# Performance work log

Measured on AMD Instinct MI355X. Metric: run time of the kernel, lower is better.

Reference implementation:

```python
import jax, jax.numpy as jnp
import numpy as np

D_MODEL = 1024

def setup_inputs() -> dict:
    key = jax.random.key(0)
    ks = jax.random.split(key, 5)
    s = 1.0 / np.sqrt(D_MODEL)  # torch Linear default init scale-ish
    x = jax.random.normal(ks[0], (4, 2048, D_MODEL), dtype=jnp.float32)
    Wq = jax.random.normal(ks[1], (D_MODEL, D_MODEL), dtype=jnp.float32) * s
    Wk = jax.random.normal(ks[2], (D_MODEL, D_MODEL), dtype=jnp.float32) * s
    Wv = jax.random.normal(ks[3], (D_MODEL, D_MODEL), dtype=jnp.float32) * s
    Wo = jax.random.normal(ks[4], (D_MODEL, D_MODEL), dtype=jnp.float32) * s
    z = jnp.zeros((D_MODEL,), dtype=jnp.float32)
    return {"x": x, "Wq": Wq, "bq": z, "Wk": Wk, "bk": z, "Wv": Wv, "bv": z, "Wo": Wo, "bo": z}

def reference(x, Wq, bq, Wk, bk, Wv, bv, Wo, bo):
    # x: (B, S, D). Single-head causal attention, dropout in eval mode (identity).
    B, S, D = x.shape
    Q = jnp.einsum('bsd,ed->bse', x, Wq) + bq
    K = jnp.einsum('bsd,ed->bse', x, Wk) + bk
    V = jnp.einsum('bsd,ed->bse', x, Wv) + bv
    scores = jnp.einsum('bqd,bkd->bqk', Q, K) / jnp.sqrt(jnp.float32(D))
    causal = jnp.tril(jnp.ones((S, S), dtype=bool))  # (S, S)
    scores = jnp.where(causal, scores, -jnp.inf)
    weights = jax.nn.softmax(scores, axis=-1)
    attended = jnp.einsum('bqk,bkd->bqd', weights, V)
    out = jnp.einsum('bsd,ed->bse', attended, Wo) + bo
    return out
```

## Files before the change

### kernel.cpp

```cpp
#include <hip/hip_runtime.h>
#include <cstdint>
#include <cstddef>


#define D_MODEL 1024
#define SEQ     2048
#define BATCH   4

typedef unsigned short u16;
typedef __bf16 bf16_t;
typedef bf16_t bf16x8 __attribute__((ext_vector_type(8)));
typedef float  f32x4  __attribute__((ext_vector_type(4)));
typedef u16    u16x4  __attribute__((ext_vector_type(4)));

__device__ __forceinline__ u16 f2bf(float x) {
  union { float f; uint32_t u; } v; v.f = x;
  uint32_t r = v.u + 0x7fffu + ((v.u >> 16) & 1u);
  return (u16)(r >> 16);
}

__device__ __forceinline__ void gload_lds16(const u16* g, u16* l) {
  __builtin_amdgcn_global_load_lds((__attribute__((address_space(1))) void*)g,
                                   (__attribute__((address_space(3))) void*)l,
                                   16, 0, 0);
}

template <bool ROWSUM>
__device__ __forceinline__ void gemm_core(const u16* __restrict__ Ablk,
                                          const u16* __restrict__ Bblk,
                                          int lda, int ldb, int ksteps64,
                                          u16* As, u16* Bs,
                                          f32x4 acc[4][4], f32x4* rs) {
  const int tid  = threadIdx.x;
  const int wave = tid >> 6, lane = tid & 63;
  const int wr = (wave >> 1) * 64, wc = (wave & 1) * 64;
  const int frow = lane & 15, kq = lane >> 4;
  int sm[4], sk[4];
#pragma unroll
  for (int t = 0; t < 4; ++t) {
    const int ch = t * 256 + tid;
    sm[t] = ch >> 3;
    sk[t] = ((ch & 7) ^ (sm[t] & 7)) * 8;
  }
  int aoff[4], boff[4];
#pragma unroll
  for (int i = 0; i < 4; ++i) {
    const int ra = wr + i * 16 + frow;
    aoff[i] = ra * 64 + ((kq ^ (ra & 7)) * 8);
    const int rb = wc + i * 16 + frow;
    boff[i] = rb * 64 + ((kq ^ (rb & 7)) * 8);
  }
  bf16x8 ones;
  if (ROWSUM) {
#pragma unroll
    for (int r = 0; r < 8; ++r) ((u16*)&ones)[r] = 0x3F80;
  }

  for (int kt = 0; kt < ksteps64; ++kt) {
    __syncthreads();
    const int kb = kt * 64;
#pragma unroll
    for (int t = 0; t < 4; ++t)
      gload_lds16(Ablk + sm[t] * lda + kb + sk[t], As + (t * 256 + tid) * 8);
#pragma unroll
    for (int t = 0; t < 4; ++t)
      gload_lds16(Bblk + sm[t] * ldb + kb + sk[t], Bs + (t * 256 + tid) * 8);
    asm volatile("s_waitcnt vmcnt(0)" ::: "memory");
    __syncthreads();

#pragma unroll
    for (int kh = 0; kh < 2; ++kh) {
      const int xo = kh * 32;
      bf16x8 af[4], bf[4];
#pragma unroll
      for (int i = 0; i < 4; ++i) af[i] = *(const bf16x8*)(As + (aoff[i] ^ xo));
#pragma unroll
      for (int j = 0; j < 4; ++j) bf[j] = *(const bf16x8*)(Bs + (boff[j] ^ xo));
#pragma unroll
      for (int i = 0; i < 4; ++i)
#pragma unroll
        for (int j = 0; j < 4; ++j)
          acc[i][j] = __builtin_amdgcn_mfma_f32_16x16x32_bf16(af[i], bf[j], acc[i][j], 0, 0, 0);
      if (ROWSUM) {
#pragma unroll
        for (int i = 0; i < 4; ++i)
          rs[i] = __builtin_amdgcn_mfma_f32_16x16x32_bf16(af[i], ones, rs[i], 0, 0, 0);
      }
    }
  }
}

__global__ __launch_bounds__(256) void cvt_kernel(const float4* __restrict__ x,
                                                  const float4* __restrict__ wq,
                                                  const float4* __restrict__ wk,
                                                  const float4* __restrict__ wv,
                                                  const float4* __restrict__ wo,
                                                  u16* __restrict__ dst) {
  const int i = blockIdx.x * 256 + threadIdx.x;
  float4 v;
  if (i < 2097152) {
    v = x[i];
  } else {
    const int j = i - 2097152;
    const int w = j >> 18;
    const float4* s = (w == 0) ? wq : (w == 1) ? wk : (w == 2) ? wv : wo;
    v = s[j & 262143];
  }
  u16x4 o = {f2bf(v.x), f2bf(v.y), f2bf(v.z), f2bf(v.w)};
  *(u16x4*)(dst + (size_t)i * 4) = o;
}

__global__ __launch_bounds__(256) void proj_qk_kernel(const u16* __restrict__ xb,
                                                      const u16* __restrict__ Wq,
                                                      const u16* __restrict__ Wk,
                                                      const float* __restrict__ bq,
                                                      const float* __restrict__ bk,
                                                      u16* __restrict__ Qb,
                                                      u16* __restrict__ Kb) {
  __shared__ __align__(16) u16 As[128 * 64];
  __shared__ __align__(16) u16 Bs[128 * 64];
  const int z = blockIdx.z;
  const u16*   W    = z ? Wk : Wq;
  const float* bias = z ? bk : bq;
  u16*         out  = z ? Kb : Qb;
  const int row0 = blockIdx.x * 128, col0 = blockIdx.y * 128;
  f32x4 acc[4][4] = {};
  gemm_core<false>(xb + (size_t)row0 * D_MODEL, W + (size_t)col0 * D_MODEL,
                   D_MODEL, D_MODEL, 16, As, Bs, acc, nullptr);
  const int lane = threadIdx.x & 63, wave = threadIdx.x >> 6;
  const int wr = (wave >> 1) * 64, wc = (wave & 1) * 64;
  const int cl = lane & 15, rl = (lane >> 4) * 4;
#pragma unroll
  for (int j = 0; j < 4; ++j) {
    const int col = col0 + wc + j * 16 + cl;
    const float bb = bias[col];
#pragma unroll
    for (int i = 0; i < 4; ++i)
#pragma unroll
      for (int r = 0; r < 4; ++r) {
        const int row = row0 + wr + i * 16 + rl + r;
        out[(size_t)row * D_MODEL + col] = f2bf(acc[i][j][r] + bb);
      }
  }
}

__global__ __launch_bounds__(256) void proj_v_kernel(const u16* __restrict__ xb,
                                                     const u16* __restrict__ Wv,
                                                     const float* __restrict__ bv,
                                                     u16* __restrict__ Vt) {
  __shared__ __align__(16) u16 As[128 * 64];
  __shared__ __align__(16) u16 Bs[128 * 64];
  const int row0 = blockIdx.x * 128, col0 = blockIdx.y * 128;
  f32x4 acc[4][4] = {};
  gemm_core<false>(xb + (size_t)row0 * D_MODEL, Wv + (size_t)col0 * D_MODEL,
                   D_MODEL, D_MODEL, 16, As, Bs, acc, nullptr);
  const int lane = threadIdx.x & 63, wave = threadIdx.x >> 6;
  const int wr = (wave >> 1) * 64, wc = (wave & 1) * 64;
  const int cl = lane & 15, rl = (lane >> 4) * 4;
  const int b = row0 >> 11;
  u16* vt = Vt + (size_t)b * D_MODEL * SEQ;
#pragma unroll
  for (int j = 0; j < 4; ++j) {
    const int col = col0 + wc + j * 16 + cl;
    const float bb = bv[col];
#pragma unroll
    for (int i = 0; i < 4; ++i) {
      const int s0 = (row0 & 2047) + wr + i * 16 + rl;
      u16x4 o = {f2bf(acc[i][j][0] + bb), f2bf(acc[i][j][1] + bb),
                 f2bf(acc[i][j][2] + bb), f2bf(acc[i][j][3] + bb)};
      *(u16x4*)(vt + (size_t)col * SEQ + s0) = o;
    }
  }
}

__global__ __launch_bounds__(256) void scores_kernel(const u16* __restrict__ Qb,
                                                     const u16* __restrict__ Kb,
                                                     u16* __restrict__ Eb) {
  const int t = blockIdx.x, b = blockIdx.z;
  int qi = (int)((sqrtf(8.0f * t + 1.0f) - 1.0f) * 0.5f);
  if ((qi + 1) * (qi + 2) / 2 <= t) ++qi;
  if (qi * (qi + 1) / 2 > t) --qi;
  const int ji = t - qi * (qi + 1) / 2;
  __shared__ __align__(16) u16 As[128 * 64];
  __shared__ __align__(16) u16 Bs[128 * 64];
  const u16* A  = Qb + (size_t)(b * SEQ + qi * 128) * D_MODEL;
  const u16* Bt = Kb + (size_t)(b * SEQ + ji * 128) * D_MODEL;
  f32x4 acc[4][4] = {};
  gemm_core<false>(A, Bt, D_MODEL, D_MODEL, 16, As, Bs, acc, nullptr);
  u16* out = Eb + (size_t)b * SEQ * SEQ;
  const int lane = threadIdx.x & 63, wave = threadIdx.x >> 6;
  const int wr = (wave >> 1) * 64, wc = (wave & 1) * 64;
  const int cl = lane & 15, rl = (lane >> 4) * 4;
#pragma unroll
  for (int i = 0; i < 4; ++i)
#pragma unroll
    for (int r = 0; r < 4; ++r) {
      const int q = qi * 128 + wr + i * 16 + rl + r;
#pragma unroll
      for (int j = 0; j < 4; ++j) {
        const int jj = ji * 128 + wc + j * 16 + cl;
        out[(size_t)q * SEQ + jj] =
            (jj <= q) ? f2bf(__expf(acc[i][j][r] * 0.03125f)) : (u16)0;
      }
    }
}

__global__ __launch_bounds__(256) void pv_kernel(const u16* __restrict__ Eb,
                                                 const u16* __restrict__ Vt,
                                                 u16* __restrict__ Ab) {
  __shared__ __align__(16) u16 As[128 * 64];
  __shared__ __align__(16) u16 Bs[128 * 64];
  const int qt = 15 - blockIdx.x, dt = blockIdx.y, b = blockIdx.z;
  const u16* A  = Eb + (size_t)b * SEQ * SEQ + (size_t)(qt * 128) * SEQ;
  const u16* Bt = Vt + (size_t)b * D_MODEL * SEQ + (size_t)(dt * 128) * SEQ;
  f32x4 acc[4][4] = {};
  f32x4 rs[4] = {};
  gemm_core<true>(A, Bt, SEQ, SEQ, (qt + 1) * 2, As, Bs, acc, rs);
  const int lane = threadIdx.x & 63, wave = threadIdx.x >> 6;
  const int wr = (wave >> 1) * 64, wc = (wave & 1) * 64;
  const int cl = lane & 15, rl = (lane >> 4) * 4;
#pragma unroll
  for (int i = 0; i < 4; ++i)
#pragma unroll
    for (int r = 0; r < 4; ++r) {
      const float invl = 1.0f / rs[i][r];
      const int row = b * SEQ + qt * 128 + wr + i * 16 + rl + r;
#pragma unroll
      for (int j = 0; j < 4; ++j) {
        const int col = dt * 128 + wc + j * 16 + cl;
        Ab[(size_t)row * D_MODEL + col] = f2bf(acc[i][j][r] * invl);
      }
    }
}

__global__ __launch_bounds__(256) void out_kernel(const u16* __restrict__ Ab,
                                                  const u16* __restrict__ Wo,
                                                  const float* __restrict__ bo,
                                                  float* __restrict__ Out) {
  __shared__ __align__(16) u16 As[128 * 64];
  __shared__ __align__(16) u16 Bs[128 * 64];
  const int row0 = blockIdx.x * 128, col0 = blockIdx.y * 128;
  f32x4 acc[4][4] = {};
  gemm_core<false>(Ab + (size_t)row0 * D_MODEL, Wo + (size_t)col0 * D_MODEL,
                   D_MODEL, D_MODEL, 16, As, Bs, acc, nullptr);
  const int lane = threadIdx.x & 63, wave = threadIdx.x >> 6;
  const int wr = (wave >> 1) * 64, wc = (wave & 1) * 64;
  const int cl = lane & 15, rl = (lane >> 4) * 4;
#pragma unroll
  for (int j = 0; j < 4; ++j) {
    const int col = col0 + wc + j * 16 + cl;
    const float bb = bo[col];
#pragma unroll
    for (int i = 0; i < 4; ++i)
#pragma unroll
      for (int r = 0; r < 4; ++r) {
        const int row = row0 + wr + i * 16 + rl + r;
        Out[(size_t)row * D_MODEL + col] = acc[i][j][r] + bb;
      }
  }
}

extern "C" void kernel_launch(void* const* d_in, const int* in_sizes, int n_in,
                              void* d_out, int out_size, void* d_ws, size_t ws_size,
                              hipStream_t stream) {
  const float* x  = (const float*)d_in[0];
  const float* Wq = (const float*)d_in[1];
  const float* bq = (const float*)d_in[2];
  const float* Wk = (const float*)d_in[3];
  const float* bk = (const float*)d_in[4];
  const float* Wv = (const float*)d_in[5];
  const float* bv = (const float*)d_in[6];
  const float* Wo = (const float*)d_in[7];
  const float* bo = (const float*)d_in[8];
  float* out = (float*)d_out;
  char* ws = (char*)d_ws;

  u16* xb = (u16*)(ws);
  u16* Wb = (u16*)(ws + (16u << 20));
  u16* Qb = (u16*)(ws + (24u << 20));
  u16* Kb = (u16*)(ws + (40u << 20));
  u16* Vt = (u16*)(ws + (56u << 20));
  u16* Eb = (u16*)(ws + (72u << 20));
  u16* Ab = (u16*)(ws + (104u << 20));

  cvt_kernel<<<12288, 256, 0, stream>>>((const float4*)x, (const float4*)Wq,
                                        (const float4*)Wk, (const float4*)Wv,
                                        (const float4*)Wo, xb);
  proj_qk_kernel<<<dim3(64, 8, 2), 256, 0, stream>>>(xb, Wb, Wb + (1u << 20),
                                                     bq, bk, Qb, Kb);
  proj_v_kernel<<<dim3(64, 8), 256, 0, stream>>>(xb, Wb + (2u << 20), bv, Vt);
  scores_kernel<<<dim3(136, 1, 4), 256, 0, stream>>>(Qb, Kb, Eb);
  pv_kernel<<<dim3(16, 8, 4), 256, 0, stream>>>(Eb, Vt, Ab);
  out_kernel<<<dim3(64, 8), 256, 0, stream>>>(Ab, Wb + (3u << 20), bo, out);
}
```

Baseline: 291.2 us.

## Fold output projection into V weights and merge stages into fewer kernels

Precomputes Wp = Wo·Wv and bp = Wo·bv so that V' = x·Wpᵀ + bp already includes the output projection. The separate out_kernel GEMM is removed and pv_kernel writes the final fp32 output plus bo directly. The QK projections are merged with the Wp computation into one launch, and the scores GEMM with the V' projection into another, to cut launch count and fill more of the GPU. The cost is an extra 1024³ weight GEMM, a transpose and an added bf16 rounding of the fused weight, which can shift accuracy.

```diff
diff --git a/kernel.cpp b/kernel.cpp
--- a/kernel.cpp
+++ b/kernel.cpp
@@ -110,104 +110,148 @@
   *(u16x4*)(dst + (size_t)i * 4) = o;
 }
 
-__global__ __launch_bounds__(256) void proj_qk_kernel(const u16* __restrict__ xb,
-                                                      const u16* __restrict__ Wq,
-                                                      const u16* __restrict__ Wk,
-                                                      const float* __restrict__ bq,
-                                                      const float* __restrict__ bk,
-                                                      u16* __restrict__ Qb,
-                                                      u16* __restrict__ Kb) {
+__global__ void transposeW_kernel(const u16* __restrict__ src, u16* __restrict__ dst) {
+  __shared__ u16 tile[32][33];
+  const int r0 = blockIdx.x * 32, c0 = blockIdx.y * 32;
+  const int tx = threadIdx.x, ty = threadIdx.y;
+#pragma unroll
+  for (int r = 0; r < 4; ++r)
+    tile[ty + r * 8][tx] = src[(size_t)(r0 + ty + r * 8) * D_MODEL + c0 + tx];
+  __syncthreads();
+#pragma unroll
+  for (int r = 0; r < 4; ++r)
+    dst[(size_t)(c0 + ty + r * 8) * D_MODEL + r0 + tx] = tile[tx][ty + r * 8];
+}
+
+__global__ __launch_bounds__(256) void stageA_kernel(
+    const u16* __restrict__ xb,
+    const u16* __restrict__ WqB, const u16* __restrict__ WkB,
+    const u16* __restrict__ WoB, const u16* __restrict__ WvT,
+    const float* __restrict__ Wo32, const float* __restrict__ bv,
+    const float* __restrict__ bq, const float* __restrict__ bk,
+    u16* __restrict__ Qb, u16* __restrict__ Kb,
+    u16* __restrict__ Wp, float* __restrict__ bp) {
   __shared__ __align__(16) u16 As[128 * 64];
   __shared__ __align__(16) u16 Bs[128 * 64];
-  const int z = blockIdx.z;
-  const u16*   W    = z ? Wk : Wq;
-  const float* bias = z ? bk : bq;
-  u16*         out  = z ? Kb : Qb;
-  const int row0 = blockIdx.x * 128, col0 = blockIdx.y * 128;
-  f32x4 acc[4][4] = {};
-  gemm_core<false>(xb + (size_t)row0 * D_MODEL, W + (size_t)col0 * D_MODEL,
-                   D_MODEL, D_MODEL, 16, As, Bs, acc, nullptr);
+  const int blk = blockIdx.x;
   const int lane = threadIdx.x & 63, wave = threadIdx.x >> 6;
   const int wr = (wave >> 1) * 64, wc = (wave & 1) * 64;
   const int cl = lane & 15, rl = (lane >> 4) * 4;
-#pragma unroll
-  for (int j = 0; j < 4; ++j) {
-    const int col = col0 + wc + j * 16 + cl;
-    const float bb = bias[col];
-#pragma unroll
-    for (int i = 0; i < 4; ++i)
-#pragma unroll
-      for (int r = 0; r < 4; ++r) {
-        const int row = row0 + wr + i * 16 + rl + r;
-        out[(size_t)row * D_MODEL + col] = f2bf(acc[i][j][r] + bb);
-      }
-  }
-}
-
-__global__ __launch_bounds__(256) void proj_v_kernel(const u16* __restrict__ xb,
-                                                     const u16* __restrict__ Wv,
-                                                     const float* __restrict__ bv,
-                                                     u16* __restrict__ Vt) {
+
+  if (blk < 64) {
+    const int f0 = (blk >> 3) * 128, e0 = (blk & 7) * 128;
+    f32x4 acc[4][4] = {};
+    gemm_core<false>(WoB + (size_t)f0 * D_MODEL, WvT + (size_t)e0 * D_MODEL,
+                     D_MODEL, D_MODEL, 16, As, Bs, acc, nullptr);
+#pragma unroll
+    for (int j = 0; j < 4; ++j) {
+      const int col = e0 + wc + j * 16 + cl;
+#pragma unroll
+      for (int i = 0; i < 4; ++i)
+#pragma unroll
+        for (int r = 0; r < 4; ++r) {
+          const int row = f0 + wr + i * 16 + rl + r;
+          Wp[(size_t)row * D_MODEL + col] = f2bf(acc[i][j][r]);
+        }
+    }
+  } else if (blk < 80) {
+    const int f = (blk - 64) * 64 + (threadIdx.x >> 2);
+    const int dq = threadIdx.x & 3;
+    const float* row = Wo32 + (size_t)f * D_MODEL + dq * 256;
+    const float* bvq = bv + dq * 256;
+    float s = 0.f;
+#pragma unroll 8
+    for (int i = 0; i < 256; ++i) s += row[i] * bvq[i];
+    s += __shfl_xor(s, 1);
+    s += __shfl_xor(s, 2);
+    if (dq == 0) bp[f] = s;
+  } else {
+    const int u = blk - 80;
+    const int z = u >> 9;
+    const u16*   W    = z ? WkB : WqB;
+    const float* bias = z ? bk : bq;
+    u16*         out  = z ? Kb : Qb;
+    const int row0 = ((u >> 3) & 63) * 128, col0 = (u & 7) * 128;
+    f32x4 acc[4][4] = {};
+    gemm_core<false>(xb + (size_t)row0 * D_MODEL, W + (size_t)col0 * D_MODEL,
+                     D_MODEL, D_MODEL, 16, As, Bs, acc, nullptr);
+#pragma unroll
+    for (int j = 0; j < 4; ++j) {
+      const int col = col0 + wc + j * 16 + cl;
+      const float bb = bias[col];
+#pragma unroll
+      for (int i = 0; i < 4; ++i)
+#pragma unroll
+        for (int r = 0; r < 4; ++r) {
+          const int row = row0 + wr + i * 16 + rl + r;
+          out[(size_t)row * D_MODEL + col] = f2bf(acc[i][j][r] + bb);
+        }
+    }
+  }
+}
+
+__global__ __launch_bounds__(256) void stageB_kernel(
+    const u16* __restrict__ xb, const u16* __restrict__ Wp,
+    const float* __restrict__ bp,
+    const u16* __restrict__ Qb, const u16* __restrict__ Kb,
+    u16* __restrict__ Vt, u16* __restrict__ Eb) {
   __shared__ __align__(16) u16 As[128 * 64];
   __shared__ __align__(16) u16 Bs[128 * 64];
-  const int row0 = blockIdx.x * 128, col0 = blockIdx.y * 128;
-  f32x4 acc[4][4] = {};
-  gemm_core<false>(xb + (size_t)row0 * D_MODEL, Wv + (size_t)col0 * D_MODEL,
-                   D_MODEL, D_MODEL, 16, As, Bs, acc, nullptr);
+  const int blk = blockIdx.x;
   const int lane = threadIdx.x & 63, wave = threadIdx.x >> 6;
   const int wr = (wave >> 1) * 64, wc = (wave & 1) * 64;
   const int cl = lane & 15, rl = (lane >> 4) * 4;
-  const int b = row0 >> 11;
-  u16* vt = Vt + (size_t)b * D_MODEL * SEQ;
-#pragma unroll
-  for (int j = 0; j < 4; ++j) {
-    const int col = col0 + wc + j * 16 + cl;
-    const float bb = bv[col];
-#pragma unroll
-    for (int i = 0; i < 4; ++i) {
-      const int s0 = (row0 & 2047) + wr + i * 16 + rl;
-      u16x4 o = {f2bf(acc[i][j][0] + bb), f2bf(acc[i][j][1] + bb),
-                 f2bf(acc[i][j][2] + bb), f2bf(acc[i][j][3] + bb)};
-      *(u16x4*)(vt + (size_t)col * SEQ + s0) = o;
-    }
-  }
-}
-
-__global__ __launch_bounds__(256) void scores_kernel(const u16* __restrict__ Qb,
-                                                     const u16* __restrict__ Kb,
-                                                     u16* __restrict__ Eb) {
-  const int t = blockIdx.x, b = blockIdx.z;
-  int qi = (int)((sqrtf(8.0f * t + 1.0f) - 1.0f) * 0.5f);
-  if ((qi + 1) * (qi + 2) / 2 <= t) ++qi;
-  if (qi * (qi + 1) / 2 > t) --qi;
-  const int ji = t - qi * (qi + 1) / 2;
-  __shared__ __align__(16) u16 As[128 * 64];
-  __shared__ __align__(16) u16 Bs[128 * 64];
-  const u16* A  = Qb + (size_t)(b * SEQ + qi * 128) * D_MODEL;
-  const u16* Bt = Kb + (size_t)(b * SEQ + ji * 128) * D_MODEL;
-  f32x4 acc[4][4] = {};
-  gemm_core<false>(A, Bt, D_MODEL, D_MODEL, 16, As, Bs, acc, nullptr);
-  u16* out = Eb + (size_t)b * SEQ * SEQ;
-  const int lane = threadIdx.x & 63, wave = threadIdx.x >> 6;
-  const int wr = (wave >> 1) * 64, wc = (wave & 1) * 64;
-  const int cl = lane & 15, rl = (lane >> 4) * 4;
-#pragma unroll
-  for (int i = 0; i < 4; ++i)
-#pragma unroll
-    for (int r = 0; r < 4; ++r) {
-      const int q = qi * 128 + wr + i * 16 + rl + r;
-#pragma unroll
-      for (int j = 0; j < 4; ++j) {
-        const int jj = ji * 128 + wc + j * 16 + cl;
-        out[(size_t)q * SEQ + jj] =
-            (jj <= q) ? f2bf(__expf(acc[i][j][r] * 0.03125f)) : (u16)0;
+
+  if (blk < 544) {
+    const int b = blk / 136, t = blk % 136;
+    int qi = (int)((sqrtf(8.0f * t + 1.0f) - 1.0f) * 0.5f);
+    if ((qi + 1) * (qi + 2) / 2 <= t) ++qi;
+    if (qi * (qi + 1) / 2 > t) --qi;
+    const int ji = t - qi * (qi + 1) / 2;
+    const u16* A  = Qb + (size_t)(b * SEQ + qi * 128) * D_MODEL;
+    const u16* Bt = Kb + (size_t)(b * SEQ + ji * 128) * D_MODEL;
+    f32x4 acc[4][4] = {};
+    gemm_core<false>(A, Bt, D_MODEL, D_MODEL, 16, As, Bs, acc, nullptr);
+    u16* out = Eb + (size_t)b * SEQ * SEQ;
+#pragma unroll
+    for (int i = 0; i < 4; ++i)
+#pragma unroll
+      for (int r = 0; r < 4; ++r) {
+        const int q = qi * 128 + wr + i * 16 + rl + r;
+#pragma unroll
+        for (int j = 0; j < 4; ++j) {
+          const int jj = ji * 128 + wc + j * 16 + cl;
+          out[(size_t)q * SEQ + jj] =
+              (jj <= q) ? f2bf(__expf(acc[i][j][r] * 0.03125f)) : (u16)0;
+        }
       }
-    }
+  } else {
+    const int u = blk - 544;
+    const int row0 = (u >> 3) * 128, col0 = (u & 7) * 128;
+    f32x4 acc[4][4] = {};
+    gemm_core<false>(xb + (size_t)row0 * D_MODEL, Wp + (size_t)col0 * D_MODEL,
+                     D_MODEL, D_MODEL, 16, As, Bs, acc, nullptr);
+    const int b = row0 >> 11;
+    u16* vt = Vt + (size_t)b * D_MODEL * SEQ;
+#pragma unroll
+    for (int j = 0; j < 4; ++j) {
+      const int col = col0 + wc + j * 16 + cl;
+      const float bb = bp[col];
+#pragma unroll
+      for (int i = 0; i < 4; ++i) {
+        const int s0 = (row0 & 2047) + wr + i * 16 + rl;
+        u16x4 o = {f2bf(acc[i][j][0] + bb), f2bf(acc[i][j][1] + bb),
+                   f2bf(acc[i][j][2] + bb), f2bf(acc[i][j][3] + bb)};
+        *(u16x4*)(vt + (size_t)col * SEQ + s0) = o;
+      }
+    }
+  }
 }
 
 __global__ __launch_bounds__(256) void pv_kernel(const u16* __restrict__ Eb,
                                                  const u16* __restrict__ Vt,
-                                                 u16* __restrict__ Ab) {
+                                                 const float* __restrict__ bo,
+                                                 float* __restrict__ Out) {
   __shared__ __align__(16) u16 As[128 * 64];
   __shared__ __align__(16) u16 Bs[128 * 64];
   const int qt = 15 - blockIdx.x, dt = blockIdx.y, b = blockIdx.z;
@@ -228,36 +272,9 @@
 #pragma unroll
       for (int j = 0; j < 4; ++j) {
         const int col = dt * 128 + wc + j * 16 + cl;
-        Ab[(size_t)row * D_MODEL + col] = f2bf(acc[i][j][r] * invl);
+        Out[(size_t)row * D_MODEL + col] = acc[i][j][r] * invl + bo[col];
       }
     }
-}
-
-__global__ __launch_bounds__(256) void out_kernel(const u16* __restrict__ Ab,
-                                                  const u16* __restrict__ Wo,
-                                                  const float* __restrict__ bo,
-                                                  float* __restrict__ Out) {
-  __shared__ __align__(16) u16 As[128 * 64];
-  __shared__ __align__(16) u16 Bs[128 * 64];
-  const int row0 = blockIdx.x * 128, col0 = blockIdx.y * 128;
-  f32x4 acc[4][4] = {};
-  gemm_core<false>(Ab + (size_t)row0 * D_MODEL, Wo + (size_t)col0 * D_MODEL,
-                   D_MODEL, D_MODEL, 16, As, Bs, acc, nullptr);
-  const int lane = threadIdx.x & 63, wave = threadIdx.x >> 6;
-  const int wr = (wave >> 1) * 64, wc = (wave & 1) * 64;
-  const int cl = lane & 15, rl = (lane >> 4) * 4;
-#pragma unroll
-  for (int j = 0; j < 4; ++j) {
-    const int col = col0 + wc + j * 16 + cl;
-    const float bb = bo[col];
-#pragma unroll
-    for (int i = 0; i < 4; ++i)
-#pragma unroll
-      for (int r = 0; r < 4; ++r) {
-        const int row = row0 + wr + i * 16 + rl + r;
-        Out[(size_t)row * D_MODEL + col] = acc[i][j][r] + bb;
-      }
-  }
 }
 
 extern "C" void kernel_launch(void* const* d_in, const int* in_sizes, int n_in,
@@ -275,21 +292,22 @@
   float* out = (float*)d_out;
   char* ws = (char*)d_ws;
 
-  u16* xb = (u16*)(ws);
-  u16* Wb = (u16*)(ws + (16u << 20));
-  u16* Qb = (u16*)(ws + (24u << 20));
-  u16* Kb = (u16*)(ws + (40u << 20));
-  u16* Vt = (u16*)(ws + (56u << 20));
-  u16* Eb = (u16*)(ws + (72u << 20));
-  u16* Ab = (u16*)(ws + (104u << 20));
+  u16*   xb  = (u16*)(ws);
+  u16*   Wb  = (u16*)(ws + (16u << 20));
+  u16*   Qb  = (u16*)(ws + (24u << 20));
+  u16*   Kb  = (u16*)(ws + (40u << 20));
+  u16*   Vt  = (u16*)(ws + (56u << 20));
+  u16*   Eb  = (u16*)(ws + (72u << 20));
+  u16*   WvT = (u16*)(ws + (104u << 20));
+  u16*   Wp  = (u16*)(ws + (106u << 20));
+  float* bp  = (float*)(ws + (108u << 20));
 
   cvt_kernel<<<12288, 256, 0, stream>>>((const float4*)x, (const float4*)Wq,
                                         (const float4*)Wk, (const float4*)Wv,
                                         (const float4*)Wo, xb);
-  proj_qk_kernel<<<dim3(64, 8, 2), 256, 0, stream>>>(xb, Wb, Wb + (1u << 20),
-                                                     bq, bk, Qb, Kb);
-  proj_v_kernel<<<dim3(64, 8), 256, 0, stream>>>(xb, Wb + (2u << 20), bv, Vt);
-  scores_kernel<<<dim3(136, 1, 4), 256, 0, stream>>>(Qb, Kb, Eb);
-  pv_kernel<<<dim3(16, 8, 4), 256, 0, stream>>>(Eb, Vt, Ab);
-  out_kernel<<<dim3(64, 8), 256, 0, stream>>>(Ab, Wb + (3u << 20), bo, out);
-}
+  transposeW_kernel<<<dim3(32, 32), dim3(32, 8), 0, stream>>>(Wb + (2u << 20), WvT);
+  stageA_kernel<<<1104, 256, 0, stream>>>(xb, Wb, Wb + (1u << 20), Wb + (3u << 20),
+                                          WvT, Wo, bv, bq, bk, Qb, Kb, Wp, bp);
+  stageB_kernel<<<1056, 256, 0, stream>>>(xb, Wp, bp, Qb, Kb, Vt, Eb);
+  pv_kernel<<<dim3(16, 8, 4), 256, 0, stream>>>(Eb, Vt, bo, out);
+}
```

After: 287.0 us. About the same (-1.4%).
